# Kernel tuning notes

Hardware: AMD Instinct MI355X
Metric: run time of the kernel (lower is better)

Reference implementation:

```python
import jax, jax.numpy as jnp
import numpy as np

# FlowNetC correlation hyperparameters (init_kwargs)
PAD = 4            # pad_size
KERNEL = 1         # kernel_size (1x1 patch)
MD = 4             # max_displacement
STRIDE1 = 1        # stride over output positions
STRIDE2 = 1        # stride over displacements


def setup_inputs() -> dict:
    key = jax.random.key(0)
    k1, k2 = jax.random.split(key)
    input1 = jax.random.normal(k1, (8, 256, 96, 128), dtype=jnp.float32)
    input2 = jax.random.normal(k2, (8, 256, 96, 128), dtype=jnp.float32)
    return {"input1": input1, "input2": input2}


def reference(input1, input2):
    # Cost volume: out[b, d, y, x] = (1/C) * sum_c input1[b,c,y,x] * input2[b,c,y+dy,x+dx]
    # for all displacements (dy, dx) in [-MD, MD] with step STRIDE2.
    # With pad_size == max_displacement, kernel_size == 1, stride1 == 1 the output
    # spatial grid equals the input grid (FlowNetC configuration). Normalization
    # matches correlation_cuda: sumelems = kernel_size^2 * C.
    B, C, H, W = input1.shape
    p2 = jnp.pad(input2, ((0, 0), (0, 0), (PAD, PAD), (PAD, PAD)))
    disp = range(-MD, MD + 1, STRIDE2)  # 9 offsets -> 81 displacement channels
    outs = []
    for dy in disp:
        for dx in disp:
            shifted = jax.lax.dynamic_slice(p2, (0, 0, PAD + dy, PAD + dx), (B, C, H, W))
            # mean over channels == sum / (KERNEL*KERNEL*C) since KERNEL == 1
            outs.append(jnp.mean(input1 * shifted, axis=1))
    return jnp.stack(outs, axis=1)  # [B, 81, H, W]
```

## Files before the change

### kernel.cpp

```cpp
#include <hip/hip_runtime.h>
#include <hip/hip_bf16.h>


#define B_ 8
#define C_ 256
#define H_ 96
#define W_ 128
#define HW_ 12288
#define CHW_ 3145728

#define IN1_OFF 0
#define IN2_OFF 8192
#define IN2_ROWB (32 * 64)

typedef __attribute__((ext_vector_type(8))) short short8;
typedef __attribute__((ext_vector_type(4))) float f32x4;

__device__ __forceinline__ int swz16(int g, int slot) {
    return (g ^ (slot & 3) ^ ((slot >> 2) & 3)) * 16;
}

__device__ __forceinline__ void stage16(const float* __restrict__ sp, char* __restrict__ base,
                                        int slot, int g) {
    f32x4 v[8];
    #pragma unroll
    for (int j = 0; j < 8; ++j) v[j] = *(const f32x4*)(sp + (size_t)j * HW_);
    #pragma unroll
    for (int p = 0; p < 4; ++p) {
        union { __hip_bfloat162 h2[4]; short8 s8; } u;
        #pragma unroll
        for (int jj = 0; jj < 4; ++jj)
            u.h2[jj] = __float22bfloat162_rn(float2{v[2 * jj][p], v[2 * jj + 1][p]});
        *(short8*)(base + (slot + p) * 64 + swz16(g, slot + p)) = u.s8;
    }
}

__global__ __launch_bounds__(512, 4) void corr_mfma3(
    const float* __restrict__ in1,
    const float* __restrict__ in2,
    float* __restrict__ out)
{
    __shared__ __align__(16) char lds[40960];

    const int tid = threadIdx.x;

    const int blk  = blockIdx.x;
    const int b    = blk & 7;
    const int rest = blk >> 3;
    const int yt   = rest >> 3;
    const int xh   = rest & 7;

    #pragma unroll
    for (int k = 0; k < 5; ++k)
        *(f32x4*)(lds + tid * 16 + k * 8192) = f32x4{0.f, 0.f, 0.f, 0.f};

    const int lane = tid & 63;
    const int wv   = tid >> 6;
    const int ut   = wv & 1;
    const int yrh  = wv >> 1;
    const int ln   = lane & 15;
    const int qd   = lane >> 4;

    const int offA0 = IN1_OFF + ((2 * yrh) * 16 + ln) * 64 + swz16(qd, ln);
    const int pB    = 16 * ut + ln;
    const int offB  = IN2_OFF + ((2 * yrh) * 32 + pB) * 64 + swz16(qd, pB);

    const float* in1b = in1 + (size_t)b * CHW_;
    const float* in2b = in2 + (size_t)b * CHW_;

    const int pp2 = tid & 7;
    const int g2  = (tid >> 3) & 3;
    const int r2  = tid >> 5;
    const int px2 = 4 * pp2;
    const int gx2 = xh * 16 - 8 + px2;
    const int ry2 = yt * 8 - 4 + r2;
    const bool valid2 = (gx2 >= 0) && (gx2 <= 124) && (ry2 >= 0) && (ry2 < H_);
    const int slot2 = r2 * 32 + px2;

    const int pp1 = tid & 3;
    const int g1  = (tid >> 2) & 3;
    const int r1  = tid >> 4;
    const int px1 = 4 * pp1;
    const int gx1 = xh * 16 + px1;
    const int y1  = yt * 8 + r1;
    const int slot1 = r1 * 16 + px1;

    f32x4 acc0[9], acc1[9];
    #pragma unroll
    for (int s = 0; s < 9; ++s) { acc0[s] = f32x4{0.f,0.f,0.f,0.f}; acc1[s] = f32x4{0.f,0.f,0.f,0.f}; }

    __syncthreads();

    for (int kc = 0; kc < 8; ++kc) {
        const size_t choff = (size_t)(kc * 32) * HW_;
        if (valid2)
            stage16(in2b + choff + (size_t)(8 * g2) * HW_ + ry2 * W_ + gx2,
                    lds + IN2_OFF, slot2, g2);
        if (tid < 128)
            stage16(in1b + choff + (size_t)(8 * g1) * HW_ + y1 * W_ + gx1,
                    lds + IN1_OFF, slot1, g1);
        __syncthreads();
        short8 a0  = *(const short8*)(lds + offA0);
        short8 a1  = *(const short8*)(lds + offA0 + 16 * 64);
        short8 blo = *(const short8*)(lds + offB);
        #pragma unroll
        for (int s = 0; s < 9; ++s) {
            short8 bhi = *(const short8*)(lds + offB + (s + 1) * IN2_ROWB);
            acc0[s] = __builtin_amdgcn_mfma_f32_16x16x32_bf16(a0, blo, acc0[s], 0, 0, 0);
            acc1[s] = __builtin_amdgcn_mfma_f32_16x16x32_bf16(a1, bhi, acc1[s], 0, 0, 0);
            blo = bhi;
        }
        __syncthreads();
    }

    const float scale = 1.0f / 256.0f;
    const int x0 = xh * 16;
    const int ybase = yt * 8 + 2 * yrh;
    #pragma unroll
    for (int s = 0; s < 9; ++s) {
        #pragma unroll
        for (int yr = 0; yr < 2; ++yr) {
            const f32x4 a = yr ? acc1[s] : acc0[s];
            const int y = ybase + yr;
            #pragma unroll
            for (int r = 0; r < 4; ++r) {
                const int m  = qd * 4 + r;
                const int dx = ln - m - 8 + 16 * ut;
                if (dx >= -4 && dx <= 4) {
                    out[(((size_t)b * 81 + (size_t)(s * 9 + dx + 4)) * H_ + y) * W_ + (x0 + m)]
                        = a[r] * scale;
                }
            }
        }
    }
}

extern "C" void kernel_launch(void* const* d_in, const int* in_sizes, int n_in,
                              void* d_out, int out_size, void* d_ws, size_t ws_size,
                              hipStream_t stream) {
    const float* in1 = (const float*)d_in[0];
    const float* in2 = (const float*)d_in[1];
    float* out = (float*)d_out;

    corr_mfma3<<<768, 512, 0, stream>>>(in1, in2, out);
}
```

Measured before the change: 262.5 us.

## Double-buffer LDS staging with register prefetch of next channel chunk

Switches to two LDS buffers. The next 32-channel chunk's global loads go into registers while the current chunk is converted to bf16, stored and consumed by MFMAs, which removes one of the two barriers per iteration. Staging of input1 is also spread across all 512 threads instead of 128. The cost is double the LDS per block and launch bounds that drop to 2 blocks per CU, so the 768-block grid may leave a partial second wave.

```diff
diff --git a/kernel.cpp b/kernel.cpp
--- a/kernel.cpp
+++ b/kernel.cpp
@@ -9,6 +9,7 @@
 #define HW_ 12288
 #define CHW_ 3145728
 
+#define BUFSZ 40960
 #define IN1_OFF 0
 #define IN2_OFF 8192
 #define IN2_ROWB (32 * 64)
@@ -20,27 +21,12 @@
     return (g ^ (slot & 3) ^ ((slot >> 2) & 3)) * 16;
 }
 
-__device__ __forceinline__ void stage16(const float* __restrict__ sp, char* __restrict__ base,
-                                        int slot, int g) {
-    f32x4 v[8];
-    #pragma unroll
-    for (int j = 0; j < 8; ++j) v[j] = *(const f32x4*)(sp + (size_t)j * HW_);
-    #pragma unroll
-    for (int p = 0; p < 4; ++p) {
-        union { __hip_bfloat162 h2[4]; short8 s8; } u;
-        #pragma unroll
-        for (int jj = 0; jj < 4; ++jj)
-            u.h2[jj] = __float22bfloat162_rn(float2{v[2 * jj][p], v[2 * jj + 1][p]});
-        *(short8*)(base + (slot + p) * 64 + swz16(g, slot + p)) = u.s8;
-    }
-}
-
-__global__ __launch_bounds__(512, 4) void corr_mfma3(
+__global__ __launch_bounds__(512, 2) void corr_mfma4(
     const float* __restrict__ in1,
     const float* __restrict__ in2,
     float* __restrict__ out)
 {
-    __shared__ __align__(16) char lds[40960];
+    __shared__ __align__(16) char lds[2 * BUFSZ];
 
     const int tid = threadIdx.x;
 
@@ -51,7 +37,7 @@
     const int xh   = rest & 7;
 
     #pragma unroll
-    for (int k = 0; k < 5; ++k)
+    for (int k = 0; k < 10; ++k)
         *(f32x4*)(lds + tid * 16 + k * 8192) = f32x4{0.f, 0.f, 0.f, 0.f};
 
     const int lane = tid & 63;
@@ -70,20 +56,54 @@
 
     const int pp2 = tid & 7;
     const int g2  = (tid >> 3) & 3;
-    const int r2  = tid >> 5;
+    const int r2i = tid >> 5;
     const int px2 = 4 * pp2;
     const int gx2 = xh * 16 - 8 + px2;
-    const int ry2 = yt * 8 - 4 + r2;
+    const int ry2 = yt * 8 - 4 + r2i;
     const bool valid2 = (gx2 >= 0) && (gx2 <= 124) && (ry2 >= 0) && (ry2 < H_);
-    const int slot2 = r2 * 32 + px2;
+    const int slot2 = r2i * 32 + px2;
+    const float* sp2base = in2b + (size_t)(8 * g2) * HW_ + ry2 * W_ + gx2;
 
-    const int pp1 = tid & 3;
-    const int g1  = (tid >> 2) & 3;
-    const int r1  = tid >> 4;
-    const int px1 = 4 * pp1;
+    const int pq1 = tid & 3;
+    const int jj1 = (tid >> 2) & 3;
+    const int g1  = (tid >> 4) & 3;
+    const int r1i = tid >> 6;
+    const int px1 = 4 * pq1;
     const int gx1 = xh * 16 + px1;
-    const int y1  = yt * 8 + r1;
-    const int slot1 = r1 * 16 + px1;
+    const int y1  = yt * 8 + r1i;
+    const int slot1 = r1i * 16 + px1;
+    const float* sp1base = in1b + (size_t)(8 * g1 + 2 * jj1) * HW_ + y1 * W_ + gx1;
+
+    f32x4 r2[8], r1v[2];
+
+    auto issue = [&](int kc) {
+        const size_t ch = (size_t)kc * 32 * HW_;
+        if (valid2) {
+            #pragma unroll
+            for (int j = 0; j < 8; ++j)
+                r2[j] = *(const f32x4*)(sp2base + ch + (size_t)j * HW_);
+        }
+        r1v[0] = *(const f32x4*)(sp1base + ch);
+        r1v[1] = *(const f32x4*)(sp1base + ch + HW_);
+    };
+
+    auto store = [&](char* __restrict__ buf) {
+        if (valid2) {
+            #pragma unroll
+            for (int p = 0; p < 4; ++p) {
+                union { __hip_bfloat162 h2[4]; short8 s8; } u;
+                #pragma unroll
+                for (int jj = 0; jj < 4; ++jj)
+                    u.h2[jj] = __float22bfloat162_rn(float2{r2[2 * jj][p], r2[2 * jj + 1][p]});
+                *(short8*)(buf + IN2_OFF + (slot2 + p) * 64 + swz16(g2, slot2 + p)) = u.s8;
+            }
+        }
+        #pragma unroll
+        for (int p = 0; p < 4; ++p) {
+            __hip_bfloat162 h = __float22bfloat162_rn(float2{r1v[0][p], r1v[1][p]});
+            *(__hip_bfloat162*)(buf + IN1_OFF + (slot1 + p) * 64 + swz16(g1, slot1 + p) + 4 * jj1) = h;
+        }
+    };
 
     f32x4 acc0[9], acc1[9];
     #pragma unroll
@@ -91,26 +111,25 @@
 
     __syncthreads();
 
+    issue(0);
+
     for (int kc = 0; kc < 8; ++kc) {
-        const size_t choff = (size_t)(kc * 32) * HW_;
-        if (valid2)
-            stage16(in2b + choff + (size_t)(8 * g2) * HW_ + ry2 * W_ + gx2,
-                    lds + IN2_OFF, slot2, g2);
-        if (tid < 128)
-            stage16(in1b + choff + (size_t)(8 * g1) * HW_ + y1 * W_ + gx1,
-                    lds + IN1_OFF, slot1, g1);
-        __syncthreads();
-        short8 a0  = *(const short8*)(lds + offA0);
-        short8 a1  = *(const short8*)(lds + offA0 + 16 * 64);
-        short8 blo = *(const short8*)(lds + offB);
+        char* buf = lds + (kc & 1) * BUFSZ;
+        store(buf);
+        if (kc < 7) issue(kc + 1);
+        asm volatile("s_waitcnt lgkmcnt(0)" ::: "memory");
+        __builtin_amdgcn_s_barrier();
+        asm volatile("" ::: "memory");
+        short8 a0  = *(const short8*)(buf + offA0);
+        short8 a1  = *(const short8*)(buf + offA0 + 16 * 64);
+        short8 blo = *(const short8*)(buf + offB);
         #pragma unroll
         for (int s = 0; s < 9; ++s) {
-            short8 bhi = *(const short8*)(lds + offB + (s + 1) * IN2_ROWB);
+            short8 bhi = *(const short8*)(buf + offB + (s + 1) * IN2_ROWB);
             acc0[s] = __builtin_amdgcn_mfma_f32_16x16x32_bf16(a0, blo, acc0[s], 0, 0, 0);
             acc1[s] = __builtin_amdgcn_mfma_f32_16x16x32_bf16(a1, bhi, acc1[s], 0, 0, 0);
             blo = bhi;
         }
-        __syncthreads();
     }
 
     const float scale = 1.0f / 256.0f;
@@ -142,5 +161,5 @@
     const float* in2 = (const float*)d_in[1];
     float* out = (float*)d_out;
 
-    corr_mfma3<<<768, 512, 0, stream>>>(in1, in2, out);
+    corr_mfma4<<<768, 512, 0, stream>>>(in1, in2, out);
 }
```

Result: faster. 251.5 us (-4.2%).
